# Optimization experiments

Measured on AMD Instinct MI355X. Metric: run time of the kernel, lower is better.

## Reference

```python
import jax, jax.numpy as jnp
import numpy as np

EPS = 1e-6

def _layernorm(x, gamma, beta):
    # normalize over last dim (head_dim)
    mean = x.mean(axis=-1, keepdims=True)
    var = x.var(axis=-1, keepdims=True)
    return gamma * (x - mean) * jax.lax.rsqrt(var + EPS) + beta

def setup_inputs() -> dict:
    key = jax.random.key(0)
    ks = jax.random.split(key, 6)
    B, N, C, H = 2, 2048, 1024, 16
    Dh = C // H
    x = jax.random.normal(ks[0], (B, N, C), dtype=jnp.float32)
    qkv_w = jax.random.normal(ks[1], (C, 3 * C), dtype=jnp.float32) * (1.0 / np.sqrt(C))
    q_gamma = jnp.ones((Dh,), jnp.float32)
    q_beta = jnp.zeros((Dh,), jnp.float32)
    k_gamma = jnp.ones((Dh,), jnp.float32)
    k_beta = jnp.zeros((Dh,), jnp.float32)
    proj_w = jax.random.normal(ks[2], (C, C), dtype=jnp.float32) * (1.0 / np.sqrt(C))
    proj_b = jnp.zeros((C,), jnp.float32)
    return {"x": x, "qkv_w": qkv_w, "q_gamma": q_gamma, "q_beta": q_beta,
            "k_gamma": k_gamma, "k_beta": k_beta, "proj_w": proj_w, "proj_b": proj_b}

def reference(x, qkv_w, q_gamma, q_beta, k_gamma, k_beta, proj_w, proj_b):
    B, N, C = x.shape
    H = 16
    Dh = C // H
    scale = Dh ** -0.5
    qkv = x @ qkv_w                                   # [B,N,3C]
    qkv = qkv.reshape(B, N, 3, H, Dh)
    q = qkv[:, :, 0].transpose(0, 2, 1, 3)            # [B,H,N,Dh]
    k = qkv[:, :, 1].transpose(0, 2, 1, 3)
    v = qkv[:, :, 2].transpose(0, 2, 1, 3)
    q = _layernorm(q, q_gamma, q_beta)
    k = _layernorm(k, k_gamma, k_beta)
    attn = jnp.einsum('bhnd,bhmd->bhnm', q, k) * scale
    attn = jax.nn.softmax(attn, axis=-1)
    out = jnp.einsum('bhnm,bhmd->bhnd', attn, v)      # [B,H,N,Dh]
    out = out.transpose(0, 2, 1, 3).reshape(B, N, C)
    return out @ proj_w + proj_b
```

## Files before the change

kernel.cpp:

```cpp
#include <hip/hip_runtime.h>

typedef unsigned short u16;
typedef unsigned int u32;
typedef float f32x4 __attribute__((ext_vector_type(4)));
typedef float f32x16 __attribute__((ext_vector_type(16)));
typedef short s16x8 __attribute__((ext_vector_type(8)));

#define B_ 2
#define N_ 2048
#define C_ 1024
#define H_ 16
#define BN_ (B_*N_)

#define EXP2F(x) __builtin_amdgcn_exp2f(x)

__device__ __forceinline__ u16 f2bf(float f) {
  union { float f; unsigned u; } c; c.f = f;
  unsigned u = c.u;
  u = (u + 0x7fffu + ((u >> 16) & 1u)) >> 16;
  return (u16)u;
}
__device__ __forceinline__ float bf2f(u16 h) {
  union { unsigned u; float f; } c; c.u = ((unsigned)h) << 16;
  return c.f;
}
__device__ __forceinline__ u32 pack2(float lo, float hi) {
  u32 r;
  asm("v_cvt_pk_bf16_f32 %0, %1, %2" : "=v"(r) : "v"(lo), "v"(hi));
  return r;
}
__device__ __forceinline__ void plswap(u32& a, u32& b) {
  asm volatile("v_permlane32_swap_b32 %0, %1" : "+v"(a), "+v"(b));
}
__device__ __forceinline__ void gload16(const u16* g, u16* l) {
  __builtin_amdgcn_global_load_lds(
      (const __attribute__((address_space(1))) unsigned*)g,
      (__attribute__((address_space(3))) unsigned*)l, 16, 0, 0);
}

__global__ __launch_bounds__(256) void k_prep(const float* __restrict__ x,
                                              u16* __restrict__ xb,
                                              const float* __restrict__ qkv_w,
                                              u16* __restrict__ wqkvT,
                                              const float* __restrict__ proj_w,
                                              u16* __restrict__ wprojT) {
  __shared__ float t[32][33];
  int bid = blockIdx.x;
  int tid = threadIdx.x;
  if (bid < 4096) {
    int i = bid * 256 + tid;
    float4 v = ((const float4*)x)[i];
    ushort4 r;
    r.x = f2bf(v.x); r.y = f2bf(v.y); r.z = f2bf(v.z); r.w = f2bf(v.w);
    ((ushort4*)xb)[i] = r;
    return;
  }
  const float* W; u16* Wt; int R, Cc, bx, by;
  if (bid < 7168) {
    int b = bid - 4096;
    bx = b % 96; by = b / 96;
    W = qkv_w; Wt = wqkvT; R = C_; Cc = 3 * C_;
  } else {
    int b = bid - 7168;
    bx = b & 31; by = b >> 5;
    W = proj_w; Wt = wprojT; R = C_; Cc = C_;
  }
  int tx = tid & 31, ty = tid >> 5;
  int c0 = bx * 32, r0 = by * 32;
#pragma unroll
  for (int i = 0; i < 4; ++i)
    t[ty + i * 8][tx] = W[(long)(r0 + ty + i * 8) * Cc + c0 + tx];
  __syncthreads();
#pragma unroll
  for (int i = 0; i < 4; ++i)
    Wt[(long)(c0 + ty + i * 8) * R + r0 + tx] = f2bf(t[tx][ty + i * 8]);
}

__global__ __launch_bounds__(256) void k_gemm_qkv_ln(const u16* __restrict__ A,
                                                     const u16* __restrict__ Bt,
                                                     const float* __restrict__ qg,
                                                     const float* __restrict__ qbeta,
                                                     const float* __restrict__ kg,
                                                     const float* __restrict__ kbeta,
                                                     u16* __restrict__ Qh,
                                                     u16* __restrict__ Kh,
                                                     u16* __restrict__ Vt) {
  const int K = C_;
  __shared__ u16 smem[18432];
  int tid = threadIdx.x;
  int w = tid >> 6, l = tid & 63;
  int l15 = l & 15, lhi = l >> 4;
  int wm = w >> 1, wn = w & 1;
  int srow = l >> 2;
  int scol = ((l & 3) ^ ((l >> 3) & 3)) * 8;
  int xo = (lhi ^ ((l15 >> 1) & 3)) * 8;
  const u16* Ab = A + (long)blockIdx.y * 128 * K;
  const u16* Bb = Bt + (long)blockIdx.x * 128 * K;
  f32x4 acc[4][4];
#pragma unroll
  for (int m = 0; m < 4; ++m)
#pragma unroll
    for (int n = 0; n < 4; ++n)
      acc[m][n] = (f32x4){0.f, 0.f, 0.f, 0.f};

  auto STAGE = [&](int k0, int bi) {
    u16* at = smem + bi * 4096;
    u16* bt = smem + 8192 + bi * 4096;
#pragma unroll
    for (int i = 0; i < 2; ++i) {
      int ri = (i * 4 + w) * 16;
      gload16(Ab + (long)(ri + srow) * K + k0 + scol, &at[ri * 32]);
      gload16(Bb + (long)(ri + srow) * K + k0 + scol, &bt[ri * 32]);
    }
  };

  const int NS = K / 32;
  STAGE(0, 0);
  for (int t = 0; t < NS; ++t) {
    __builtin_amdgcn_s_barrier();
    if (t + 1 < NS) {
      STAGE((t + 1) * 32, (t + 1) & 1);
      asm volatile("s_waitcnt vmcnt(4)" ::: "memory");
    } else {
      asm volatile("s_waitcnt vmcnt(0)" ::: "memory");
    }
    __builtin_amdgcn_s_barrier();
    const u16* at = smem + (t & 1) * 4096;
    const u16* bt = smem + 8192 + (t & 1) * 4096;
    s16x8 af[4], bfr[4];
#pragma unroll
    for (int m = 0; m < 4; ++m)
      af[m] = *(const s16x8*)&at[(wm * 64 + m * 16 + l15) * 32 + xo];
#pragma unroll
    for (int n = 0; n < 4; ++n)
      bfr[n] = *(const s16x8*)&bt[(wn * 64 + n * 16 + l15) * 32 + xo];
#pragma unroll
    for (int m = 0; m < 4; ++m)
#pragma unroll
      for (int n = 0; n < 4; ++n)
        acc[m][n] = __builtin_amdgcn_mfma_f32_16x16x32_bf16(af[m], bfr[n], acc[m][n], 0, 0, 0);
  }

  int cb = blockIdx.x * 128 + wn * 64;
  int s = cb >> 10;
  int h = (cb & 1023) >> 6;
  int rowbase = blockIdx.y * 128 + wm * 64;

  if (s == 2) {
    __syncthreads();
    u16* tbuf = smem + w * 4608;
    u32* tb32 = (u32*)tbuf;
#pragma unroll
    for (int m = 0; m < 4; ++m)
#pragma unroll
      for (int n = 0; n < 4; ++n) {
        int d = n * 16 + l15;
#pragma unroll
        for (int r = 0; r < 4; r += 2)
          tb32[d * 36 + m * 8 + lhi * 2 + (r >> 1)] =
              pack2(acc[m][n][r], acc[m][n][r + 1]);
      }
    int b = rowbase >> 11;
    int nnb = rowbase & (N_ - 1);
    int bhv = b * H_ + h;
    int ch = (l & 7) * 8;
#pragma unroll
    for (int i = 0; i < 8; ++i) {
      int dl = i * 8 + (l >> 3);
      s16x8 vv = *(const s16x8*)&tbuf[dl * 72 + ch];
      *(s16x8*)&Vt[(long)(bhv * 64 + dl) * N_ + nnb + ch] = vv;
    }
  } else {
    const float* g = (s == 0) ? qg : kg;
    const float* be = (s == 0) ? qbeta : kbeta;
    u16* Oh = (s == 0) ? Qh : Kh;
    float sc = (s == 0) ? 0.125f * 1.44269504089f : 1.f;
    float gv[4], bv[4];
#pragma unroll
    for (int n = 0; n < 4; ++n) { gv[n] = g[n * 16 + l15]; bv[n] = be[n * 16 + l15]; }
#pragma unroll
    for (int m = 0; m < 4; ++m) {
#pragma unroll
      for (int r = 0; r < 4; ++r) {
        float t = (acc[m][0][r] + acc[m][1][r]) + (acc[m][2][r] + acc[m][3][r]);
        t += __shfl_xor(t, 1); t += __shfl_xor(t, 2);
        t += __shfl_xor(t, 4); t += __shfl_xor(t, 8);
        float mean = t * (1.f / 64.f);
        float v0 = acc[m][0][r] - mean, v1 = acc[m][1][r] - mean;
        float v2 = acc[m][2][r] - mean, v3 = acc[m][3][r] - mean;
        float q2 = (v0 * v0 + v1 * v1) + (v2 * v2 + v3 * v3);
        q2 += __shfl_xor(q2, 1); q2 += __shfl_xor(q2, 2);
        q2 += __shfl_xor(q2, 4); q2 += __shfl_xor(q2, 8);
        float rs = rsqrtf(q2 * (1.f / 64.f) + 1e-6f);
        int row = rowbase + m * 16 + lhi * 4 + r;
        int b = row >> 11, nn = row & (N_ - 1);
        long ob = ((long)(b * H_ + h) * N_ + nn) * 64;
        float vv[4] = {v0, v1, v2, v3};
#pragma unroll
        for (int n = 0; n < 4; ++n)
          Oh[ob + n * 16 + l15] = f2bf(sc * (gv[n] * vv[n] * rs + bv[n]));
      }
    }
  }
}

__global__ __launch_bounds__(256) void k_gemm_proj(const u16* __restrict__ A,
                                                   const u16* __restrict__ Bt,
                                                   float* __restrict__ Cout,
                                                   const float* __restrict__ bias,
                                                   int M, int N, int K) {
  __shared__ u16 a_t[2][128 * 64];
  __shared__ u16 b_t[2][128 * 64];
  int tid = threadIdx.x;
  int w = tid >> 6, l = tid & 63;
  int l15 = l & 15, lhi = l >> 4;
  int wm = w >> 1, wn = w & 1;
  int rowA = l >> 3;
  int colA = ((l & 7) ^ (rowA & 7)) * 8;
  int x0 = (lhi ^ (l15 & 7)) * 8;
  int x1 = ((4 + lhi) ^ (l15 & 7)) * 8;
  const u16* Ab = A + (long)blockIdx.y * 128 * K;
  const u16* Bb = Bt + (long)blockIdx.x * 128 * K;
  f32x4 acc[4][4];
#pragma unroll
  for (int m = 0; m < 4; ++m)
#pragma unroll
    for (int n = 0; n < 4; ++n)
      acc[m][n] = (f32x4){0.f, 0.f, 0.f, 0.f};

  auto STAGE = [&](int k0, int bi) {
#pragma unroll
    for (int i = 0; i < 4; ++i) {
      int ci = i * 4 + w;
      gload16(Ab + (long)(ci * 8 + rowA) * K + k0 + colA, &a_t[bi][ci * 512]);
      gload16(Bb + (long)(ci * 8 + rowA) * K + k0 + colA, &b_t[bi][ci * 512]);
    }
  };

  const int NS = 1024 / 64;
  STAGE(0, 0);
  for (int t = 0; t < NS; ++t) {
    __builtin_amdgcn_s_barrier();
    if (t + 1 < NS) {
      STAGE((t + 1) * 64, (t + 1) & 1);
      asm volatile("s_waitcnt vmcnt(8)" ::: "memory");
    } else {
      asm volatile("s_waitcnt vmcnt(0)" ::: "memory");
    }
    __builtin_amdgcn_s_barrier();
    const u16* at = a_t[t & 1];
    const u16* bt = b_t[t & 1];
#pragma unroll
    for (int kk = 0; kk < 2; ++kk) {
      int xo = kk ? x1 : x0;
      s16x8 af[4], bfr[4];
#pragma unroll
      for (int m = 0; m < 4; ++m)
        af[m] = *(const s16x8*)&at[(wm * 64 + m * 16 + l15) * 64 + xo];
#pragma unroll
      for (int n = 0; n < 4; ++n)
        bfr[n] = *(const s16x8*)&bt[(wn * 64 + n * 16 + l15) * 64 + xo];
#pragma unroll
      for (int m = 0; m < 4; ++m)
#pragma unroll
        for (int n = 0; n < 4; ++n)
          acc[m][n] = __builtin_amdgcn_mfma_f32_16x16x32_bf16(af[m], bfr[n], acc[m][n], 0, 0, 0);
    }
  }
#pragma unroll
  for (int m = 0; m < 4; ++m) {
#pragma unroll
    for (int n = 0; n < 4; ++n) {
      int col = blockIdx.x * 128 + wn * 64 + n * 16 + l15;
#pragma unroll
      for (int r = 0; r < 4; ++r) {
        int row = blockIdx.y * 128 + wm * 64 + m * 16 + lhi * 4 + r;
        Cout[(long)row * N + col] = acc[m][n][r] + bias[col];
      }
    }
  }
}

__global__ __launch_bounds__(512, 4) void k_attn(const u16* __restrict__ Qh,
                                                 const u16* __restrict__ Kh,
                                                 const u16* __restrict__ Vt,
                                                 u16* __restrict__ O) {
  __shared__ u16 k_t[2][2][64 * 64];
  __shared__ u16 v_t[2][2][64 * 64];
  int tid = threadIdx.x;
  int w = tid >> 6, l = tid & 63;
  int half = w >> 2, wq = w & 3;
  int l31 = l & 31, hi = l >> 5;
  int id = blockIdx.x;
  int swz = (id & 7) * 64 + (id >> 3);
  int bh = swz >> 4, qb = swz & 15;
  int b = bh >> 4, h = bh & 15;
  const u16* Qb = Qh + ((long)bh * N_ + qb * 128 + wq * 32) * 64;
  const u16* Kb = Kh + ((long)bh * N_ + half * 1024) * 64;
  const u16* Vb = Vt + (long)bh * 64 * N_ + half * 1024;

  s16x8 qf[4];
#pragma unroll
  for (int j = 0; j < 4; ++j)
    qf[j] = *(const s16x8*)&Qb[l31 * 64 + j * 16 + hi * 8];

  f32x16 acc0, acc1;
#pragma unroll
  for (int i = 0; i < 16; ++i) { acc0[i] = 0.f; acc1[i] = 0.f; }
  float lsum = 0.f;

  int off[2][4];
#pragma unroll
  for (int t = 0; t < 2; ++t)
#pragma unroll
    for (int j = 0; j < 4; ++j)
      off[t][j] = (t * 32 + l31) * 64 + (((j * 2 + hi) ^ (l & 7)) * 8);

  int srow = l >> 3;
  int scol = ((l & 7) ^ srow) * 8;

  auto STAGE = [&](int kt, int bi) {
#pragma unroll
    for (int i = 0; i < 2; ++i) {
      int ci = i * 4 + wq;
      gload16(Kb + (long)(kt + ci * 8 + srow) * 64 + scol, &k_t[half][bi][ci * 512]);
      gload16(Vb + (long)(ci * 8 + srow) * N_ + kt + scol, &v_t[half][bi][ci * 512]);
    }
  };

  const int NT = 16;
  STAGE(0, 0);

  for (int t = 0; t < NT; ++t) {
    __builtin_amdgcn_s_barrier();
    if (t + 1 < NT) {
      STAGE((t + 1) * 64, (t + 1) & 1);
      asm volatile("s_waitcnt vmcnt(4)" ::: "memory");
    } else {
      asm volatile("s_waitcnt vmcnt(0)" ::: "memory");
    }
    __builtin_amdgcn_s_barrier();
    const u16* kb = k_t[half][t & 1];
    const u16* vb = v_t[half][t & 1];

    f32x16 s0, s1;
#pragma unroll
    for (int i = 0; i < 16; ++i) { s0[i] = 0.f; s1[i] = 0.f; }
    __builtin_amdgcn_s_setprio(1);
#pragma unroll
    for (int j = 0; j < 4; ++j) {
      s16x8 kf0 = *(const s16x8*)&kb[off[0][j]];
      s0 = __builtin_amdgcn_mfma_f32_32x32x16_bf16(kf0, qf[j], s0, 0, 0, 0);
      s16x8 kf1 = *(const s16x8*)&kb[off[1][j]];
      s1 = __builtin_amdgcn_mfma_f32_32x32x16_bf16(kf1, qf[j], s1, 0, 0, 0);
    }
    __builtin_amdgcn_s_setprio(0);

#pragma unroll
    for (int i = 0; i < 16; ++i) {
      s0[i] = EXP2F(s0[i]);
      s1[i] = EXP2F(s1[i]);
    }
    f32x16 sm;
#pragma unroll
    for (int i = 0; i < 16; ++i) sm[i] = s0[i] + s1[i];
#pragma unroll
    for (int i = 0; i < 8; ++i) sm[i] += sm[i + 8];
#pragma unroll
    for (int i = 0; i < 4; ++i) sm[i] += sm[i + 4];
    lsum += (sm[0] + sm[1]) + (sm[2] + sm[3]);

    s16x8 pa[4];
#pragma unroll
    for (int g = 0; g < 4; ++g) {
      const f32x16& sv = (g < 2) ? s0 : s1;
      int o = (g & 1) * 8;
      u32 a = pack2(sv[o + 0], sv[o + 1]);
      u32 bb = pack2(sv[o + 4], sv[o + 5]);
      u32 c = pack2(sv[o + 2], sv[o + 3]);
      u32 d = pack2(sv[o + 6], sv[o + 7]);
      plswap(a, bb);
      plswap(c, d);
      union { u32 u[4]; s16x8 v; } fr;
      fr.u[0] = a; fr.u[1] = c; fr.u[2] = bb; fr.u[3] = d;
      pa[g] = fr.v;
    }

    __builtin_amdgcn_s_setprio(1);
#pragma unroll
    for (int j = 0; j < 4; ++j) {
      s16x8 vf0 = *(const s16x8*)&vb[off[0][j]];
      acc0 = __builtin_amdgcn_mfma_f32_32x32x16_bf16(pa[j], vf0, acc0, 0, 0, 0);
      s16x8 vf1 = *(const s16x8*)&vb[off[1][j]];
      acc1 = __builtin_amdgcn_mfma_f32_32x32x16_bf16(pa[j], vf1, acc1, 0, 0, 0);
    }
    __builtin_amdgcn_s_setprio(0);
  }

  lsum += __shfl_xor(lsum, 32);

  __syncthreads();
  float* mbuf = (float*)&k_t[0][0][0];
  float* ml   = (float*)&v_t[0][0][0];

  if (half == 1) {
    if (hi == 0) ml[wq * 32 + l31] = lsum;
#pragma unroll
    for (int r = 0; r < 16; ++r) {
      mbuf[((wq * 32 + r) * 64) + l] = acc0[r];
      mbuf[((wq * 32 + 16 + r) * 64) + l] = acc1[r];
    }
  }
  __syncthreads();

  if (half == 0) {
    float s_b = ml[wq * 32 + l31];
    float lstar = lsum + s_b;
    int lsi = __float_as_int(lstar);
#pragma unroll
    for (int r = 0; r < 16; ++r) {
      int ql = (r & 3) + 8 * (r >> 2) + 4 * hi;
      float ls = __int_as_float(__builtin_amdgcn_ds_bpermute(ql << 2, lsi));
      float o0 = acc0[r] + mbuf[((wq * 32 + r) * 64) + l];
      float o1 = acc1[r] + mbuf[((wq * 32 + 16 + r) * 64) + l];
      float inv = 1.f / ls;
      int q = qb * 128 + wq * 32 + ql;
      long ob = ((long)(b * N_ + q) * H_ + h) * 64 + l31;
      O[ob] = f2bf(o0 * inv);
      O[ob + 32] = f2bf(o1 * inv);
    }
  }
}

extern "C" void kernel_launch(void* const* d_in, const int* in_sizes, int n_in,
                              void* d_out, int out_size, void* d_ws, size_t ws_size,
                              hipStream_t stream) {
  const float* x      = (const float*)d_in[0];
  const float* qkv_w  = (const float*)d_in[1];
  const float* q_g    = (const float*)d_in[2];
  const float* q_b    = (const float*)d_in[3];
  const float* k_g    = (const float*)d_in[4];
  const float* k_b    = (const float*)d_in[5];
  const float* proj_w = (const float*)d_in[6];
  const float* proj_b = (const float*)d_in[7];
  float* out = (float*)d_out;

  char* ws = (char*)d_ws;
  u16* xb     = (u16*)(ws + 0);
  u16* wqkvT  = (u16*)(ws + 8388608);
  u16* wprojT = (u16*)(ws + 14680064);
  u16* Qh     = (u16*)(ws + 16777216);
  u16* Kh     = (u16*)(ws + 25165824);
  u16* Vt     = (u16*)(ws + 41943040);
  u16* attnO  = xb;

  k_prep<<<8192, 256, 0, stream>>>(x, xb, qkv_w, wqkvT, proj_w, wprojT);
  k_gemm_qkv_ln<<<dim3(24, 32), 256, 0, stream>>>(xb, wqkvT, q_g, q_b, k_g, k_b, Qh, Kh, Vt);
  k_attn<<<512, 512, 0, stream>>>(Qh, Kh, Vt, attnO);
  k_gemm_proj<<<dim3(8, 32), 256, 0, stream>>>(attnO, wprojT, out, proj_b, BN_, C_, C_);
}
```

Before: 122.0 us.

## Deepen QKV GEMM K-tile to 64 and halve proj GEMM N-tile

The QKV GEMM now stages 64-wide K slices with an 8-way XOR swizzle, matching the proj GEMM layout. This halves the number of barrier-separated iterations and doubles the MFMA work per stage, at the cost of more shared memory. The proj GEMM moves from 128x128 to 128x64 tiles, doubling the grid to 512 blocks so more CUs stay busy. That gives up some operand reuse per block. The epilogue smem reuse in the QKV kernel must still fit within the enlarged buffer.

```diff
diff --git a/kernel.cpp b/kernel.cpp
--- a/kernel.cpp
+++ b/kernel.cpp
@@ -86,14 +86,15 @@
                                                      u16* __restrict__ Kh,
                                                      u16* __restrict__ Vt) {
   const int K = C_;
-  __shared__ u16 smem[18432];
+  __shared__ u16 smem[32768];
   int tid = threadIdx.x;
   int w = tid >> 6, l = tid & 63;
   int l15 = l & 15, lhi = l >> 4;
   int wm = w >> 1, wn = w & 1;
-  int srow = l >> 2;
-  int scol = ((l & 3) ^ ((l >> 3) & 3)) * 8;
-  int xo = (lhi ^ ((l15 >> 1) & 3)) * 8;
+  int rowA = l >> 3;
+  int colA = ((l & 7) ^ (rowA & 7)) * 8;
+  int x0 = (lhi ^ (l15 & 7)) * 8;
+  int x1 = ((4 + lhi) ^ (l15 & 7)) * 8;
   const u16* Ab = A + (long)blockIdx.y * 128 * K;
   const u16* Bb = Bt + (long)blockIdx.x * 128 * K;
   f32x4 acc[4][4];
@@ -104,41 +105,45 @@
       acc[m][n] = (f32x4){0.f, 0.f, 0.f, 0.f};
 
   auto STAGE = [&](int k0, int bi) {
-    u16* at = smem + bi * 4096;
-    u16* bt = smem + 8192 + bi * 4096;
-#pragma unroll
-    for (int i = 0; i < 2; ++i) {
-      int ri = (i * 4 + w) * 16;
-      gload16(Ab + (long)(ri + srow) * K + k0 + scol, &at[ri * 32]);
-      gload16(Bb + (long)(ri + srow) * K + k0 + scol, &bt[ri * 32]);
+    u16* at = smem + bi * 8192;
+    u16* bt = smem + 16384 + bi * 8192;
+#pragma unroll
+    for (int i = 0; i < 4; ++i) {
+      int ci = i * 4 + w;
+      gload16(Ab + (long)(ci * 8 + rowA) * K + k0 + colA, &at[ci * 512]);
+      gload16(Bb + (long)(ci * 8 + rowA) * K + k0 + colA, &bt[ci * 512]);
     }
   };
 
-  const int NS = K / 32;
+  const int NS = K / 64;
   STAGE(0, 0);
   for (int t = 0; t < NS; ++t) {
     __builtin_amdgcn_s_barrier();
     if (t + 1 < NS) {
-      STAGE((t + 1) * 32, (t + 1) & 1);
-      asm volatile("s_waitcnt vmcnt(4)" ::: "memory");
+      STAGE((t + 1) * 64, (t + 1) & 1);
+      asm volatile("s_waitcnt vmcnt(8)" ::: "memory");
     } else {
       asm volatile("s_waitcnt vmcnt(0)" ::: "memory");
     }
     __builtin_amdgcn_s_barrier();
-    const u16* at = smem + (t & 1) * 4096;
-    const u16* bt = smem + 8192 + (t & 1) * 4096;
-    s16x8 af[4], bfr[4];
-#pragma unroll
-    for (int m = 0; m < 4; ++m)
-      af[m] = *(const s16x8*)&at[(wm * 64 + m * 16 + l15) * 32 + xo];
-#pragma unroll
-    for (int n = 0; n < 4; ++n)
-      bfr[n] = *(const s16x8*)&bt[(wn * 64 + n * 16 + l15) * 32 + xo];
-#pragma unroll
-    for (int m = 0; m < 4; ++m)
+    const u16* at = smem + (t & 1) * 8192;
+    const u16* bt = smem + 16384 + (t & 1) * 8192;
+#pragma unroll
+    for (int kk = 0; kk < 2; ++kk) {
+      int xo = kk ? x1 : x0;
+      s16x8 af[4], bfr[4];
+#pragma unroll
+      for (int m = 0; m < 4; ++m)
+        af[m] = *(const s16x8*)&at[(wm * 64 + m * 16 + l15) * 64 + xo];
 #pragma unroll
       for (int n = 0; n < 4; ++n)
-        acc[m][n] = __builtin_amdgcn_mfma_f32_16x16x32_bf16(af[m], bfr[n], acc[m][n], 0, 0, 0);
+        bfr[n] = *(const s16x8*)&bt[(wn * 64 + n * 16 + l15) * 64 + xo];
+#pragma unroll
+      for (int m = 0; m < 4; ++m)
+#pragma unroll
+        for (int n = 0; n < 4; ++n)
+          acc[m][n] = __builtin_amdgcn_mfma_f32_16x16x32_bf16(af[m], bfr[n], acc[m][n], 0, 0, 0);
+    }
   }
 
   int cb = blockIdx.x * 128 + wn * 64;
@@ -210,20 +215,19 @@
                                                    const float* __restrict__ bias,
                                                    int M, int N, int K) {
   __shared__ u16 a_t[2][128 * 64];
-  __shared__ u16 b_t[2][128 * 64];
+  __shared__ u16 b_t[2][64 * 64];
   int tid = threadIdx.x;
   int w = tid >> 6, l = tid & 63;
   int l15 = l & 15, lhi = l >> 4;
-  int wm = w >> 1, wn = w & 1;
   int rowA = l >> 3;
   int colA = ((l & 7) ^ (rowA & 7)) * 8;
   int x0 = (lhi ^ (l15 & 7)) * 8;
   int x1 = ((4 + lhi) ^ (l15 & 7)) * 8;
   const u16* Ab = A + (long)blockIdx.y * 128 * K;
-  const u16* Bb = Bt + (long)blockIdx.x * 128 * K;
-  f32x4 acc[4][4];
-#pragma unroll
-  for (int m = 0; m < 4; ++m)
+  const u16* Bb = Bt + (long)blockIdx.x * 64 * K;
+  f32x4 acc[2][4];
+#pragma unroll
+  for (int m = 0; m < 2; ++m)
 #pragma unroll
     for (int n = 0; n < 4; ++n)
       acc[m][n] = (f32x4){0.f, 0.f, 0.f, 0.f};
@@ -233,6 +237,10 @@
     for (int i = 0; i < 4; ++i) {
       int ci = i * 4 + w;
       gload16(Ab + (long)(ci * 8 + rowA) * K + k0 + colA, &a_t[bi][ci * 512]);
+    }
+#pragma unroll
+    for (int i = 0; i < 2; ++i) {
+      int ci = i * 4 + w;
       gload16(Bb + (long)(ci * 8 + rowA) * K + k0 + colA, &b_t[bi][ci * 512]);
     }
   };
@@ -243,7 +251,7 @@
     __builtin_amdgcn_s_barrier();
     if (t + 1 < NS) {
       STAGE((t + 1) * 64, (t + 1) & 1);
-      asm volatile("s_waitcnt vmcnt(8)" ::: "memory");
+      asm volatile("s_waitcnt vmcnt(6)" ::: "memory");
     } else {
       asm volatile("s_waitcnt vmcnt(0)" ::: "memory");
     }
@@ -253,28 +261,28 @@
 #pragma unroll
     for (int kk = 0; kk < 2; ++kk) {
       int xo = kk ? x1 : x0;
-      s16x8 af[4], bfr[4];
-#pragma unroll
-      for (int m = 0; m < 4; ++m)
-        af[m] = *(const s16x8*)&at[(wm * 64 + m * 16 + l15) * 64 + xo];
+      s16x8 af[2], bfr[4];
+#pragma unroll
+      for (int m = 0; m < 2; ++m)
+        af[m] = *(const s16x8*)&at[(w * 32 + m * 16 + l15) * 64 + xo];
 #pragma unroll
       for (int n = 0; n < 4; ++n)
-        bfr[n] = *(const s16x8*)&bt[(wn * 64 + n * 16 + l15) * 64 + xo];
-#pragma unroll
-      for (int m = 0; m < 4; ++m)
+        bfr[n] = *(const s16x8*)&bt[(n * 16 + l15) * 64 + xo];
+#pragma unroll
+      for (int m = 0; m < 2; ++m)
 #pragma unroll
         for (int n = 0; n < 4; ++n)
           acc[m][n] = __builtin_amdgcn_mfma_f32_16x16x32_bf16(af[m], bfr[n], acc[m][n], 0, 0, 0);
     }
   }
 #pragma unroll
-  for (int m = 0; m < 4; ++m) {
+  for (int m = 0; m < 2; ++m) {
 #pragma unroll
     for (int n = 0; n < 4; ++n) {
-      int col = blockIdx.x * 128 + wn * 64 + n * 16 + l15;
+      int col = blockIdx.x * 64 + n * 16 + l15;
 #pragma unroll
       for (int r = 0; r < 4; ++r) {
-        int row = blockIdx.y * 128 + wm * 64 + m * 16 + lhi * 4 + r;
+        int row = blockIdx.y * 128 + w * 32 + m * 16 + lhi * 4 + r;
         Cout[(long)row * N + col] = acc[m][n][r] + bias[col];
       }
     }
@@ -457,5 +465,5 @@
   k_prep<<<8192, 256, 0, stream>>>(x, xb, qkv_w, wqkvT, proj_w, wprojT);
   k_gemm_qkv_ln<<<dim3(24, 32), 256, 0, stream>>>(xb, wqkvT, q_g, q_b, k_g, k_b, Qh, Kh, Vt);
   k_attn<<<512, 512, 0, stream>>>(Qh, Kh, Vt, attnO);
-  k_gemm_proj<<<dim3(8, 32), 256, 0, stream>>>(attnO, wprojT, out, proj_b, BN_, C_, C_);
-}
+  k_gemm_proj<<<dim3(16, 32), 256, 0, stream>>>(attnO, wprojT, out, proj_b, BN_, C_, C_);
+}
```

New measurement: 112.8 us (median of 3 runs). 1.08x faster.
